# Performance work log

Hardware: AMD Instinct MI355X
Metric: run time of the kernel (lower is better)

## Reference

```python
import jax, jax.numpy as jnp
import numpy as np

L, B, X_DIM, Y_DIM, Q_DIM, NUM_D, LR = 1024, 16, 512, 512, 64, 4, 4
H_LOW = X_DIM // LR  # low-rank bottleneck width (128)


def setup_inputs() -> dict:
    key = jax.random.key(0)
    ks = jax.random.split(key, 6)
    sx = 1.0 / np.sqrt(X_DIM)
    sh = 1.0 / np.sqrt(H_LOW)
    return {
        "input_X": jax.random.normal(ks[0], (L, B, X_DIM), dtype=jnp.float32),
        "src_mask": jnp.zeros((L, L), dtype=jnp.float32),
        # num_D independent Linear(X_dim, q_dim) projections, stacked
        "Wq": jax.random.normal(ks[1], (NUM_D, Q_DIM, X_DIM), dtype=jnp.float32) * sx,
        "bq": jax.random.normal(ks[2], (NUM_D, Q_DIM), dtype=jnp.float32) * sx,
        # NL_signal path: Linear(X_dim, X_dim//LR) -> sigmoid -> Linear(X_dim//LR, Y_dim)
        "Wh": jax.random.normal(ks[3], (H_LOW, X_DIM), dtype=jnp.float32) * sx,
        "bh": jnp.zeros((H_LOW,), dtype=jnp.float32),
        "Ws": jax.random.normal(ks[4], (Y_DIM, H_LOW), dtype=jnp.float32) * sh,
        "bs": jnp.zeros((Y_DIM,), dtype=jnp.float32),
    }


def _pairwise_l2(Q):
    # Q: [d, b, l, q] -> Euclidean cdist [d, b, l, l] via GEMM identity (p_norm = 2)
    sq = jnp.sum(Q * Q, axis=-1)  # [d, b, l]
    d2 = sq[..., :, None] + sq[..., None, :] - 2.0 * jnp.einsum('dbiq,dbjq->dbij', Q, Q)
    d2 = jnp.maximum(d2, 0.0)
    safe = jnp.where(d2 > 0, d2, 1.0)  # avoid sqrt-grad blowup at exact zeros (diagonal)
    return jnp.where(d2 > 0, jnp.sqrt(safe), 0.0)


def reference(input_X, src_mask, Wq, bq, Wh, bh, Ws, bs):
    # Qins: [num_D, L, B, q_dim]
    Qins = jnp.einsum('lbx,dqx->dlbq', input_X, Wq) + bq[:, None, None, :]
    Qt = jnp.transpose(Qins, (0, 2, 1, 3))  # [d, b, l, q]
    dist = _pairwise_l2(Qt)                  # [d, b, l, l]
    # alternating-sign coefficients (-1)**d, combine groups
    coeffs = (-1.0) ** jnp.arange(NUM_D, dtype=jnp.float32)
    relMat = jnp.einsum('dbij,d->bij', dist, coeffs) / np.sqrt(X_DIM).astype(np.float32)
    relMat = jax.nn.softmax(relMat + src_mask[None, :, :], axis=-1)  # softmax over dim 2
    # NL_signal=True, NLS_use_act=True: sigmoid low-rank bottleneck
    h = jax.nn.sigmoid(input_X @ Wh.T + bh)  # [L, B, H_LOW]
    Sin = h @ Ws.T + bs                       # [L, B, Y_DIM]
    Sout = jnp.einsum('bij,jby->biy', relMat, Sin)  # [B, L, Y_DIM]
    # temp_Qins: mean of Qins over (num_D, L) -> [B, q_dim]
    temp_Qins = jnp.mean(Qins, axis=(0, 1))
    return (Sout, temp_Qins)
```

## Files before the change

kernel.cpp:

```cpp
#include <hip/hip_runtime.h>

typedef __bf16 bf16x8 __attribute__((ext_vector_type(8)));
typedef float f32x4 __attribute__((ext_vector_type(4)));

__device__ __forceinline__ unsigned short f2bf_bits(float f) {
    unsigned int u = __builtin_bit_cast(unsigned int, f);
    u += 0x7fffu + ((u >> 16) & 1u);
    return (unsigned short)(u >> 16);
}
__device__ __forceinline__ float bf2f(unsigned short b) {
    return __builtin_bit_cast(float, (unsigned int)b << 16);
}
__device__ __forceinline__ bf16x8 ld8(const unsigned short* p) {
    return __builtin_bit_cast(bf16x8, *reinterpret_cast<const uint4*>(p));
}
__device__ __forceinline__ f32x4 mfma16(bf16x8 a, bf16x8 b, f32x4 c) {
    return __builtin_amdgcn_mfma_f32_16x16x32_bf16(a, b, c, 0, 0, 0);
}
__device__ __forceinline__ void gload16(const unsigned short* g, unsigned short* lds) {
    __builtin_amdgcn_global_load_lds(
        (const __attribute__((address_space(1))) unsigned int*)g,
        (__attribute__((address_space(3))) unsigned int*)lds, 16, 0, 0);
}

__global__ __launch_bounds__(256) void cvt_all(const float* __restrict__ X,
                                               const float* __restrict__ Wq,
                                               const float* __restrict__ Wh,
                                               const float* __restrict__ Ws,
                                               const float* __restrict__ bq,
                                               const float* __restrict__ bh,
                                               unsigned short* __restrict__ Xb,
                                               unsigned short* __restrict__ Wqhb,
                                               unsigned short* __restrict__ Wsb,
                                               float* __restrict__ biasQH) {
    const int blk = blockIdx.x;
    const float* in;
    unsigned short* out;
    int i;
    if (blk < 8192) { in = X; out = Xb; i = blk * 1024 + threadIdx.x * 4; }
    else if (blk < 8320) { in = Wq; out = Wqhb; i = (blk - 8192) * 1024 + threadIdx.x * 4; }
    else if (blk < 8384) { in = Wh; out = Wqhb + 256 * 512; i = (blk - 8320) * 1024 + threadIdx.x * 4; }
    else if (blk < 8448) { in = Ws; out = Wsb; i = (blk - 8384) * 1024 + threadIdx.x * 4; }
    else if (blk == 8448) { biasQH[threadIdx.x] = bq[threadIdx.x]; return; }
    else { if (threadIdx.x < 128) biasQH[256 + threadIdx.x] = bh[threadIdx.x]; return; }
    float4 v = *reinterpret_cast<const float4*>(in + i);
    ushort4 o;
    o.x = f2bf_bits(v.x); o.y = f2bf_bits(v.y);
    o.z = f2bf_bits(v.z); o.w = f2bf_bits(v.w);
    *reinterpret_cast<ushort4*>(out + i) = o;
}

__global__ __launch_bounds__(256) void qstats(const unsigned short* __restrict__ Qbf,
                                              float* __restrict__ sqout,
                                              float* __restrict__ part) {
    const size_t rbase = ((size_t)(blockIdx.x >> 2) << 10) + ((blockIdx.x & 3) << 8);
    {
        const size_t row = rbase + threadIdx.x;
        const uint4* p = reinterpret_cast<const uint4*>(Qbf + row * 64);
        float s = 0.f;
#pragma unroll
        for (int c = 0; c < 8; c++) {
            uint4 u = p[c];
            unsigned int w4[4] = {u.x, u.y, u.z, u.w};
#pragma unroll
            for (int k = 0; k < 4; k++) {
                float lo = __builtin_bit_cast(float, w4[k] << 16);
                float hi = __builtin_bit_cast(float, w4[k] & 0xffff0000u);
                s += lo * lo + hi * hi;
            }
        }
        sqout[row] = s;
    }
    const int q = threadIdx.x & 63, seg = threadIdx.x >> 6;
    const unsigned short* p = Qbf + (rbase + seg * 64) * 64 + q;
    float m = 0.f;
#pragma unroll 8
    for (int i = 0; i < 64; i++) m += bf2f(p[(size_t)i * 64]);
    __shared__ float red[4][64];
    red[seg][q] = m;
    __syncthreads();
    if (threadIdx.x < 64)
        part[(size_t)blockIdx.x * 64 + threadIdx.x] =
            red[0][threadIdx.x] + red[1][threadIdx.x] + red[2][threadIdx.x] + red[3][threadIdx.x];
}
__global__ __launch_bounds__(256) void qmean_comb(const float* __restrict__ part,
                                                  float* __restrict__ out2) {
    int t = blockIdx.x * 256 + threadIdx.x;
    int b = t >> 6, q = t & 63;
    float s = 0.f;
#pragma unroll
    for (int d = 0; d < 4; d++)
#pragma unroll
        for (int qt = 0; qt < 4; qt++)
            s += part[(size_t)(((d * 16 + b) << 2) + qt) * 64 + q];
    out2[t] = s * (1.f / 4096.f);
}

template <int K, int EPI>
__global__ __launch_bounds__(256) void tile_gemm(const unsigned short* __restrict__ A,
                                                 const unsigned short* __restrict__ BT,
                                                 const float* __restrict__ bias,
                                                 const float* __restrict__ lsum,
                                                 void* __restrict__ outv,
                                                 unsigned short* __restrict__ out2, int N,
                                                 size_t strideAz, size_t strideBz) {
    __shared__ unsigned short As[2][128 * 32];
    __shared__ unsigned short Bs[2][128 * 32];
    const int bm = blockIdx.x * 128, bn = blockIdx.y * 128, z = blockIdx.z;
    const unsigned short* Ap = A + (size_t)z * strideAz;
    const unsigned short* Bp = BT + (size_t)z * strideBz;
    const int tid = threadIdx.x, w = tid >> 6, l = tid & 63;
    const int lrow = l & 15, lk8 = (l >> 4) << 3, r4 = (l >> 4) << 2;
    const int wr = (w >> 1) * 64, wc = (w & 1) * 64;
    const int srow = l >> 2, scol = (l & 3) * 8;
    f32x4 acc[4][4] = {};

    auto stage = [&](int buf, int k0) {
        gload16(Ap + (size_t)(bm + w * 32 + srow) * K + k0 + scol, &As[buf][(w * 32) * 32]);
        gload16(Ap + (size_t)(bm + w * 32 + 16 + srow) * K + k0 + scol,
                &As[buf][(w * 32 + 16) * 32]);
        gload16(Bp + (size_t)(bn + w * 32 + srow) * K + k0 + scol, &Bs[buf][(w * 32) * 32]);
        gload16(Bp + (size_t)(bn + w * 32 + 16 + srow) * K + k0 + scol,
                &Bs[buf][(w * 32 + 16) * 32]);
    };

    stage(0, 0);
    __syncthreads();
    int cur = 0;
    const int NKT = K / 32;
    for (int kt = 0; kt < NKT; kt++) {
        if (kt + 1 < NKT) stage(cur ^ 1, (kt + 1) * 32);
        bf16x8 af[4], bfr[4];
#pragma unroll
        for (int t = 0; t < 4; t++) {
            af[t] = *reinterpret_cast<const bf16x8*>(&As[cur][(wr + t * 16 + lrow) * 32 + lk8]);
            bfr[t] = *reinterpret_cast<const bf16x8*>(&Bs[cur][(wc + t * 16 + lrow) * 32 + lk8]);
        }
#pragma unroll
        for (int at = 0; at < 4; at++)
#pragma unroll
            for (int bt = 0; bt < 4; bt++) acc[at][bt] = mfma16(af[at], bfr[bt], acc[at][bt]);
        __syncthreads();
        cur ^= 1;
    }
#pragma unroll
    for (int at = 0; at < 4; at++) {
        const int i = bm + wr + at * 16 + r4;
        if constexpr (EPI == 0) {
            float* out = (float*)outv;
            float inv[4];
#pragma unroll
            for (int r = 0; r < 4; r++) {
                const size_t row = (size_t)z * 1024 + i + r;
                float s = 0.f;
#pragma unroll
                for (int k = 0; k < 16; k++) s += lsum[(size_t)k * 16384 + row];
                inv[r] = 1.f / s;
            }
#pragma unroll
            for (int bt = 0; bt < 4; bt++) {
                const int y = bn + wc + bt * 16 + lrow;
#pragma unroll
                for (int r = 0; r < 4; r++)
                    out[((size_t)z * 1024 + i + r) * 512 + y] = acc[at][bt][r] * inv[r];
            }
        } else {
            unsigned short* out = (unsigned short*)outv;
#pragma unroll
            for (int bt = 0; bt < 4; bt++) {
                const int col = bn + wc + bt * 16 + lrow;
                const float bv = bias[col];
#pragma unroll
                for (int r = 0; r < 4; r++) {
                    const int row = i + r;
                    float v = acc[at][bt][r] + bv;
                    if constexpr (EPI == 3) {
                        out[(size_t)row * N + col] = f2bf_bits(v);
                    } else {
                        if (col < 256) {
                            const int d = col >> 6, q = col & 63, lidx = row >> 4, bb = row & 15;
                            out[(((size_t)(d * 16 + bb) << 10) + lidx) * 64 + q] = f2bf_bits(v);
                        } else {
                            float sv = 1.f / (1.f + __expf(-v));
                            out2[(size_t)row * 128 + (col - 256)] = f2bf_bits(sv);
                        }
                    }
                }
            }
        }
    }
}

__global__ __launch_bounds__(256) void transpose_sin(const unsigned short* __restrict__ Sinb,
                                                     unsigned short* __restrict__ SinT) {
    __shared__ unsigned short t[64][65];
    const int l0 = blockIdx.x * 64, y0 = blockIdx.y * 64, b = blockIdx.z;
    const int lane = threadIdx.x & 63, wv = threadIdx.x >> 6;
#pragma unroll
    for (int it = 0; it < 16; it++) {
        int ty = wv * 16 + it;
        t[ty][lane] = Sinb[((size_t)(l0 + ty) * 16 + b) * 512 + y0 + lane];
    }
    __syncthreads();
    const int tx4 = lane & 15, ry0 = lane >> 4;
#pragma unroll
    for (int it = 0; it < 4; it++) {
        int y = wv * 16 + it * 4 + ry0;
        ushort4 v;
        v.x = t[tx4 * 4 + 0][y];
        v.y = t[tx4 * 4 + 1][y];
        v.z = t[tx4 * 4 + 2][y];
        v.w = t[tx4 * 4 + 3][y];
        *reinterpret_cast<ushort4*>(&SinT[((size_t)b * 512 + y0 + y) * 1024 + l0 + tx4 * 4]) = v;
    }
}

__global__ __launch_bounds__(256) void score_wave(const unsigned short* __restrict__ Qbf,
                                                  const float* __restrict__ sq,
                                                  unsigned short* __restrict__ P,
                                                  float* __restrict__ lsum) {
    const int gw = blockIdx.x * 4 + (threadIdx.x >> 6);
    const int l = threadIdx.x & 63;
    const int ti = gw & 31;
    const int b = (gw >> 5) & 15;
    const int jc = gw >> 9;
    const int i0 = ti << 5;
    const int J = jc << 6;
    const int lrow = l & 15, lk8 = (l >> 4) << 3, r4 = (l >> 4) << 2;

    size_t base[4];
    bf16x8 qi[4][2][2];
    float sqi[4][2];
#pragma unroll
    for (int d = 0; d < 4; d++) {
        base[d] = ((size_t)(d * 16 + b)) << 10;
#pragma unroll
        for (int it = 0; it < 2; it++) {
            const unsigned short* p = Qbf + (base[d] + i0 + it * 16 + lrow) * 64 + lk8;
            qi[d][it][0] = ld8(p);
            qi[d][it][1] = ld8(p + 32);
            sqi[d][it] = sq[base[d] + i0 + it * 16 + lrow];
        }
    }

    const float inv_sx = 0.04419417382415922f;
    float rs[2] = {0.f, 0.f};

    bf16x8 qj[2][4][2];
#pragma unroll
    for (int d = 0; d < 4; d++) {
        const unsigned short* qjp = Qbf + (base[d] + J + lrow) * 64 + lk8;
        qj[0][d][0] = ld8(qjp);
        qj[0][d][1] = ld8(qjp + 32);
    }

#pragma unroll
    for (int t = 0; t < 4; t++) {
        const int j0 = J + t * 16;
        const int cb = t & 1;
        if (t < 3) {
            const int nb = cb ^ 1;
#pragma unroll
            for (int d = 0; d < 4; d++) {
                const unsigned short* qjp = Qbf + (base[d] + j0 + 16 + lrow) * 64 + lk8;
                qj[nb][d][0] = ld8(qjp);
                qj[nb][d][1] = ld8(qjp + 32);
            }
        }
        f32x4 sqj[4];
#pragma unroll
        for (int d = 0; d < 4; d++)
            sqj[d] = *reinterpret_cast<const f32x4*>(&sq[base[d] + j0 + r4]);
        f32x4 sacc[2][4] = {};
#pragma unroll
        for (int d = 0; d < 4; d++) {
            sacc[0][d] = mfma16(qj[cb][d][0], qi[d][0][0], sacc[0][d]);
            sacc[0][d] = mfma16(qj[cb][d][1], qi[d][0][1], sacc[0][d]);
            sacc[1][d] = mfma16(qj[cb][d][0], qi[d][1][0], sacc[1][d]);
            sacc[1][d] = mfma16(qj[cb][d][1], qi[d][1][1], sacc[1][d]);
        }
#pragma unroll
        for (int it = 0; it < 2; it++) {
            float pv[4];
#pragma unroll
            for (int r = 0; r < 4; r++) {
                float s = 0.f;
#pragma unroll
                for (int d = 0; d < 4; d++) {
                    float d2 = fmaxf(sqj[d][r] + sqi[d][it] - 2.f * sacc[it][d][r], 0.f);
                    float dist = __builtin_amdgcn_sqrtf(d2);
                    s += (d & 1) ? -dist : dist;
                }
                pv[r] = __expf(s * inv_sx);
            }
            rs[it] += (pv[0] + pv[1]) + (pv[2] + pv[3]);
            unsigned int lo, hi;
            asm("v_cvt_pk_bf16_f32 %0, %1, %2" : "=v"(lo) : "v"(pv[0]), "v"(pv[1]));
            asm("v_cvt_pk_bf16_f32 %0, %1, %2" : "=v"(hi) : "v"(pv[2]), "v"(pv[3]));
            uint2 st;
            st.x = lo;
            st.y = hi;
            *reinterpret_cast<uint2*>(
                P + (((size_t)(b << 10) + i0 + it * 16 + lrow) << 10) + j0 + r4) = st;
        }
    }
    rs[0] += __shfl_xor(rs[0], 16);
    rs[0] += __shfl_xor(rs[0], 32);
    rs[1] += __shfl_xor(rs[1], 16);
    rs[1] += __shfl_xor(rs[1], 32);
    if (l < 16) {
        lsum[(size_t)jc * 16384 + ((size_t)b << 10) + i0 + l] = rs[0];
        lsum[(size_t)jc * 16384 + ((size_t)b << 10) + i0 + 16 + l] = rs[1];
    }
}

extern "C" void kernel_launch(void* const* d_in, const int* in_sizes, int n_in,
                              void* d_out, int out_size, void* d_ws, size_t ws_size,
                              hipStream_t stream) {
    const float* X = (const float*)d_in[0];
    const float* Wq = (const float*)d_in[2];
    const float* bq = (const float*)d_in[3];
    const float* Wh = (const float*)d_in[4];
    const float* bh = (const float*)d_in[5];
    const float* Ws = (const float*)d_in[6];
    const float* bs = (const float*)d_in[7];
    float* out = (float*)d_out;

    char* ws = (char*)d_ws;
    size_t off = 0;
    auto alloc = [&](size_t bytes) {
        void* p = ws + off;
        off = (off + bytes + 255) & ~(size_t)255;
        return p;
    };
    unsigned short* Xb = (unsigned short*)alloc(16384UL * 512 * 2);
    unsigned short* Wqhb = (unsigned short*)alloc(384UL * 512 * 2);
    unsigned short* Wsb = (unsigned short*)alloc(512UL * 128 * 2);
    float* biasQH = (float*)alloc(384UL * 4);
    unsigned short* Qbf = (unsigned short*)alloc(4UL * 16 * 1024 * 64 * 2);
    float* sqb = (float*)alloc(4UL * 16 * 1024 * 4);
    unsigned short* Hb = (unsigned short*)alloc(16384UL * 128 * 2);
    unsigned short* Sinb = (unsigned short*)alloc(16384UL * 512 * 2);
    unsigned short* SinT = (unsigned short*)alloc(16UL * 512 * 1024 * 2);
    unsigned short* P = (unsigned short*)alloc(16UL * 1024 * 1024 * 2);
    float* lsum = (float*)alloc(16UL * 16384 * 4);
    float* qpart = (float*)alloc(256UL * 64 * 4);

    cvt_all<<<8450, 256, 0, stream>>>(X, Wq, Wh, Ws, bq, bh, Xb, Wqhb, Wsb, biasQH);
    tile_gemm<512, 4><<<dim3(128, 3, 1), 256, 0, stream>>>(Xb, Wqhb, biasQH, nullptr, Qbf, Hb,
                                                           384, 0, 0);
    qstats<<<256, 256, 0, stream>>>(Qbf, sqb, qpart);
    qmean_comb<<<4, 256, 0, stream>>>(qpart, out + 8388608);
    tile_gemm<128, 3><<<dim3(128, 4, 1), 256, 0, stream>>>(Hb, Wsb, bs, nullptr, Sinb, nullptr,
                                                           512, 0, 0);
    transpose_sin<<<dim3(16, 8, 16), 256, 0, stream>>>(Sinb, SinT);
    score_wave<<<2048, 256, 0, stream>>>(Qbf, sqb, P, lsum);
    tile_gemm<1024, 0><<<dim3(8, 4, 16), 256, 0, stream>>>(
        P, SinT, nullptr, lsum, out, nullptr, 512, 1024UL * 1024, 512UL * 1024);
}
```

Before: 226.6 us.

## Fuse fp32-to-bf16 conversion into GEMM staging and coalesce score stores via LDS

Drops the separate cvt_all kernel. The first two GEMMs now load fp32 X and weights straight into registers, pack them to bf16 and write the result to LDS, which removes the 16MB X→bf16 round trip through global memory. The score kernel now stages each wave's bf16 P tile in LDS and writes full 16-byte rows to global memory instead of scattered 8-byte stores. The cost is register-staged loads in place of direct global-to-LDS loads, plus extra LDS traffic and LDS footprint in score_wave.

```diff
diff --git a/kernel.cpp b/kernel.cpp
--- a/kernel.cpp
+++ b/kernel.cpp
@@ -11,6 +11,11 @@
 __device__ __forceinline__ float bf2f(unsigned short b) {
     return __builtin_bit_cast(float, (unsigned int)b << 16);
 }
+__device__ __forceinline__ unsigned int pk2(float a, float b) {
+    unsigned int r;
+    asm("v_cvt_pk_bf16_f32 %0, %1, %2" : "=v"(r) : "v"(a), "v"(b));
+    return r;
+}
 __device__ __forceinline__ bf16x8 ld8(const unsigned short* p) {
     return __builtin_bit_cast(bf16x8, *reinterpret_cast<const uint4*>(p));
 }
@@ -21,33 +26,6 @@
     __builtin_amdgcn_global_load_lds(
         (const __attribute__((address_space(1))) unsigned int*)g,
         (__attribute__((address_space(3))) unsigned int*)lds, 16, 0, 0);
-}
-
-__global__ __launch_bounds__(256) void cvt_all(const float* __restrict__ X,
-                                               const float* __restrict__ Wq,
-                                               const float* __restrict__ Wh,
-                                               const float* __restrict__ Ws,
-                                               const float* __restrict__ bq,
-                                               const float* __restrict__ bh,
-                                               unsigned short* __restrict__ Xb,
-                                               unsigned short* __restrict__ Wqhb,
-                                               unsigned short* __restrict__ Wsb,
-                                               float* __restrict__ biasQH) {
-    const int blk = blockIdx.x;
-    const float* in;
-    unsigned short* out;
-    int i;
-    if (blk < 8192) { in = X; out = Xb; i = blk * 1024 + threadIdx.x * 4; }
-    else if (blk < 8320) { in = Wq; out = Wqhb; i = (blk - 8192) * 1024 + threadIdx.x * 4; }
-    else if (blk < 8384) { in = Wh; out = Wqhb + 256 * 512; i = (blk - 8320) * 1024 + threadIdx.x * 4; }
-    else if (blk < 8448) { in = Ws; out = Wsb; i = (blk - 8384) * 1024 + threadIdx.x * 4; }
-    else if (blk == 8448) { biasQH[threadIdx.x] = bq[threadIdx.x]; return; }
-    else { if (threadIdx.x < 128) biasQH[256 + threadIdx.x] = bh[threadIdx.x]; return; }
-    float4 v = *reinterpret_cast<const float4*>(in + i);
-    ushort4 o;
-    o.x = f2bf_bits(v.x); o.y = f2bf_bits(v.y);
-    o.z = f2bf_bits(v.z); o.w = f2bf_bits(v.w);
-    *reinterpret_cast<ushort4*>(out + i) = o;
 }
 
 __global__ __launch_bounds__(256) void qstats(const unsigned short* __restrict__ Qbf,
@@ -96,10 +74,12 @@
     out2[t] = s * (1.f / 4096.f);
 }
 
-template <int K, int EPI>
-__global__ __launch_bounds__(256) void tile_gemm(const unsigned short* __restrict__ A,
-                                                 const unsigned short* __restrict__ BT,
+template <int K, int EPI, int AF, int BF>
+__global__ __launch_bounds__(256) void tile_gemm(const void* __restrict__ Av,
+                                                 const void* __restrict__ Bv,
+                                                 const void* __restrict__ B2v,
                                                  const float* __restrict__ bias,
+                                                 const float* __restrict__ bias2,
                                                  const float* __restrict__ lsum,
                                                  void* __restrict__ outv,
                                                  unsigned short* __restrict__ out2, int N,
@@ -107,29 +87,76 @@
     __shared__ unsigned short As[2][128 * 32];
     __shared__ unsigned short Bs[2][128 * 32];
     const int bm = blockIdx.x * 128, bn = blockIdx.y * 128, z = blockIdx.z;
-    const unsigned short* Ap = A + (size_t)z * strideAz;
-    const unsigned short* Bp = BT + (size_t)z * strideBz;
     const int tid = threadIdx.x, w = tid >> 6, l = tid & 63;
     const int lrow = l & 15, lk8 = (l >> 4) << 3, r4 = (l >> 4) << 2;
     const int wr = (w >> 1) * 64, wc = (w & 1) * 64;
-    const int srow = l >> 2, scol = (l & 3) * 8;
+    const int srow_g = l >> 2, scol_g = (l & 3) * 8;
+    const int srow_r = tid >> 1, scol_r = (tid & 1) * 16;
     f32x4 acc[4][4] = {};
-
-    auto stage = [&](int buf, int k0) {
-        gload16(Ap + (size_t)(bm + w * 32 + srow) * K + k0 + scol, &As[buf][(w * 32) * 32]);
-        gload16(Ap + (size_t)(bm + w * 32 + 16 + srow) * K + k0 + scol,
-                &As[buf][(w * 32 + 16) * 32]);
-        gload16(Bp + (size_t)(bn + w * 32 + srow) * K + k0 + scol, &Bs[buf][(w * 32) * 32]);
-        gload16(Bp + (size_t)(bn + w * 32 + 16 + srow) * K + k0 + scol,
-                &Bs[buf][(w * 32 + 16) * 32]);
+    float4 ra[4], rb[4];
+
+    auto issue = [&](int k0, int buf) {
+        if constexpr (AF == 0) {
+            const unsigned short* Ap = (const unsigned short*)Av + (size_t)z * strideAz;
+            gload16(Ap + (size_t)(bm + w * 32 + srow_g) * K + k0 + scol_g,
+                    &As[buf][(w * 32) * 32]);
+            gload16(Ap + (size_t)(bm + w * 32 + 16 + srow_g) * K + k0 + scol_g,
+                    &As[buf][(w * 32 + 16) * 32]);
+        } else {
+            const float* s = (const float*)Av + (size_t)(bm + srow_r) * K + k0 + scol_r;
+            ra[0] = *reinterpret_cast<const float4*>(s);
+            ra[1] = *reinterpret_cast<const float4*>(s + 4);
+            ra[2] = *reinterpret_cast<const float4*>(s + 8);
+            ra[3] = *reinterpret_cast<const float4*>(s + 12);
+        }
+        if constexpr (BF == 0) {
+            const unsigned short* Bp = (const unsigned short*)Bv + (size_t)z * strideBz;
+            gload16(Bp + (size_t)(bn + w * 32 + srow_g) * K + k0 + scol_g,
+                    &Bs[buf][(w * 32) * 32]);
+            gload16(Bp + (size_t)(bn + w * 32 + 16 + srow_g) * K + k0 + scol_g,
+                    &Bs[buf][(w * 32 + 16) * 32]);
+        } else {
+            const int row = bn + srow_r;
+            const float* s;
+            if constexpr (EPI == 4)
+                s = (row < 256 ? (const float*)Bv + (size_t)row * K
+                               : (const float*)B2v + (size_t)(row - 256) * K) + k0 + scol_r;
+            else
+                s = (const float*)Bv + (size_t)row * K + k0 + scol_r;
+            rb[0] = *reinterpret_cast<const float4*>(s);
+            rb[1] = *reinterpret_cast<const float4*>(s + 4);
+            rb[2] = *reinterpret_cast<const float4*>(s + 8);
+            rb[3] = *reinterpret_cast<const float4*>(s + 12);
+        }
     };
-
-    stage(0, 0);
+    auto commit = [&](int buf) {
+        if constexpr (AF == 1) {
+            uint4 w0, w1;
+            w0.x = pk2(ra[0].x, ra[0].y); w0.y = pk2(ra[0].z, ra[0].w);
+            w0.z = pk2(ra[1].x, ra[1].y); w0.w = pk2(ra[1].z, ra[1].w);
+            w1.x = pk2(ra[2].x, ra[2].y); w1.y = pk2(ra[2].z, ra[2].w);
+            w1.z = pk2(ra[3].x, ra[3].y); w1.w = pk2(ra[3].z, ra[3].w);
+            *reinterpret_cast<uint4*>(&As[buf][srow_r * 32 + scol_r]) = w0;
+            *reinterpret_cast<uint4*>(&As[buf][srow_r * 32 + scol_r + 8]) = w1;
+        }
+        if constexpr (BF == 1) {
+            uint4 w0, w1;
+            w0.x = pk2(rb[0].x, rb[0].y); w0.y = pk2(rb[0].z, rb[0].w);
+            w0.z = pk2(rb[1].x, rb[1].y); w0.w = pk2(rb[1].z, rb[1].w);
+            w1.x = pk2(rb[2].x, rb[2].y); w1.y = pk2(rb[2].z, rb[2].w);
+            w1.z = pk2(rb[3].x, rb[3].y); w1.w = pk2(rb[3].z, rb[3].w);
+            *reinterpret_cast<uint4*>(&Bs[buf][srow_r * 32 + scol_r]) = w0;
+            *reinterpret_cast<uint4*>(&Bs[buf][srow_r * 32 + scol_r + 8]) = w1;
+        }
+    };
+
+    issue(0, 0);
+    commit(0);
     __syncthreads();
     int cur = 0;
     const int NKT = K / 32;
     for (int kt = 0; kt < NKT; kt++) {
-        if (kt + 1 < NKT) stage(cur ^ 1, (kt + 1) * 32);
+        if (kt + 1 < NKT) issue((kt + 1) * 32, cur ^ 1);
         bf16x8 af[4], bfr[4];
 #pragma unroll
         for (int t = 0; t < 4; t++) {
@@ -140,6 +167,7 @@
         for (int at = 0; at < 4; at++)
 #pragma unroll
             for (int bt = 0; bt < 4; bt++) acc[at][bt] = mfma16(af[at], bfr[bt], acc[at][bt]);
+        if (kt + 1 < NKT) commit(cur ^ 1);
         __syncthreads();
         cur ^= 1;
     }
@@ -169,7 +197,8 @@
 #pragma unroll
             for (int bt = 0; bt < 4; bt++) {
                 const int col = bn + wc + bt * 16 + lrow;
-                const float bv = bias[col];
+                const float bv = (EPI == 4) ? (col < 256 ? bias[col] : bias2[col - 256])
+                                            : bias[col];
 #pragma unroll
                 for (int r = 0; r < 4; r++) {
                     const int row = i + r;
@@ -219,7 +248,9 @@
                                                   const float* __restrict__ sq,
                                                   unsigned short* __restrict__ P,
                                                   float* __restrict__ lsum) {
-    const int gw = blockIdx.x * 4 + (threadIdx.x >> 6);
+    __shared__ unsigned short Pt[4][32 * 88];
+    const int w = threadIdx.x >> 6;
+    const int gw = blockIdx.x * 4 + w;
     const int l = threadIdx.x & 63;
     const int ti = gw & 31;
     const int b = (gw >> 5) & 15;
@@ -227,6 +258,7 @@
     const int i0 = ti << 5;
     const int J = jc << 6;
     const int lrow = l & 15, lk8 = (l >> 4) << 3, r4 = (l >> 4) << 2;
+    unsigned short* T = &Pt[w][0];
 
     size_t base[4];
     bf16x8 qi[4][2][2];
@@ -294,15 +326,17 @@
                 pv[r] = __expf(s * inv_sx);
             }
             rs[it] += (pv[0] + pv[1]) + (pv[2] + pv[3]);
-            unsigned int lo, hi;
-            asm("v_cvt_pk_bf16_f32 %0, %1, %2" : "=v"(lo) : "v"(pv[0]), "v"(pv[1]));
-            asm("v_cvt_pk_bf16_f32 %0, %1, %2" : "=v"(hi) : "v"(pv[2]), "v"(pv[3]));
             uint2 st;
-            st.x = lo;
-            st.y = hi;
-            *reinterpret_cast<uint2*>(
-                P + (((size_t)(b << 10) + i0 + it * 16 + lrow) << 10) + j0 + r4) = st;
-        }
+            st.x = pk2(pv[0], pv[1]);
+            st.y = pk2(pv[2], pv[3]);
+            *reinterpret_cast<uint2*>(&T[(it * 16 + lrow) * 88 + t * 16 + r4]) = st;
+        }
+    }
+#pragma unroll
+    for (int k = 0; k < 4; k++) {
+        const int ri = k * 8 + (l >> 3), c = l & 7;
+        uint4 v = *reinterpret_cast<const uint4*>(&T[ri * 88 + c * 8]);
+        *reinterpret_cast<uint4*>(P + ((((size_t)(b << 10)) + i0 + ri) << 10) + J + c * 8) = v;
     }
     rs[0] += __shfl_xor(rs[0], 16);
     rs[0] += __shfl_xor(rs[0], 32);
@@ -333,10 +367,6 @@
         off = (off + bytes + 255) & ~(size_t)255;
         return p;
     };
-    unsigned short* Xb = (unsigned short*)alloc(16384UL * 512 * 2);
-    unsigned short* Wqhb = (unsigned short*)alloc(384UL * 512 * 2);
-    unsigned short* Wsb = (unsigned short*)alloc(512UL * 128 * 2);
-    float* biasQH = (float*)alloc(384UL * 4);
     unsigned short* Qbf = (unsigned short*)alloc(4UL * 16 * 1024 * 64 * 2);
     float* sqb = (float*)alloc(4UL * 16 * 1024 * 4);
     unsigned short* Hb = (unsigned short*)alloc(16384UL * 128 * 2);
@@ -346,15 +376,15 @@
     float* lsum = (float*)alloc(16UL * 16384 * 4);
     float* qpart = (float*)alloc(256UL * 64 * 4);
 
-    cvt_all<<<8450, 256, 0, stream>>>(X, Wq, Wh, Ws, bq, bh, Xb, Wqhb, Wsb, biasQH);
-    tile_gemm<512, 4><<<dim3(128, 3, 1), 256, 0, stream>>>(Xb, Wqhb, biasQH, nullptr, Qbf, Hb,
-                                                           384, 0, 0);
+    tile_gemm<512, 4, 1, 1><<<dim3(128, 3, 1), 256, 0, stream>>>(
+        X, Wq, Wh, bq, bh, nullptr, Qbf, Hb, 384, 0, 0);
     qstats<<<256, 256, 0, stream>>>(Qbf, sqb, qpart);
     qmean_comb<<<4, 256, 0, stream>>>(qpart, out + 8388608);
-    tile_gemm<128, 3><<<dim3(128, 4, 1), 256, 0, stream>>>(Hb, Wsb, bs, nullptr, Sinb, nullptr,
-                                                           512, 0, 0);
+    tile_gemm<128, 3, 0, 1><<<dim3(128, 4, 1), 256, 0, stream>>>(
+        Hb, Ws, nullptr, bs, nullptr, nullptr, Sinb, nullptr, 512, 0, 0);
     transpose_sin<<<dim3(16, 8, 16), 256, 0, stream>>>(Sinb, SinT);
     score_wave<<<2048, 256, 0, stream>>>(Qbf, sqb, P, lsum);
-    tile_gemm<1024, 0><<<dim3(8, 4, 16), 256, 0, stream>>>(
-        P, SinT, nullptr, lsum, out, nullptr, 512, 1024UL * 1024, 512UL * 1024);
-}
+    tile_gemm<1024, 0, 0, 0><<<dim3(8, 4, 16), 256, 0, stream>>>(
+        P, SinT, nullptr, nullptr, nullptr, lsum, out, nullptr, 512, 1024UL * 1024,
+        512UL * 1024);
+}
```

Measured after the change: 229.5 us. Within noise of the previous version (+1.3%).
